# Performance work log

Hardware: AMD Instinct MI355X
Metric: run time of the kernel (lower is better)

The kernel has to match this reference:

```python
import jax, jax.numpy as jnp
from jax import lax
import numpy as np

DN = ('NCHW', 'OIHW', 'NCHW')


def _gaussian_kernel1d(ksize, sigma):
    # torchvision GaussianBlur kernel: linspace-centered, normalized pdf
    x = jnp.linspace(-(ksize - 1) * 0.5, (ksize - 1) * 0.5, ksize, dtype=jnp.float32)
    pdf = jnp.exp(-0.5 * (x / sigma) ** 2)
    return pdf / pdf.sum()


def gaussian_blur(x, ksize, sigma):
    # x: [B, 1, H, W]. Separable blur with reflect padding (== torchvision
    # GaussianBlur, whose 2D kernel is the outer product of the 1D kernel).
    k = _gaussian_kernel1d(ksize, sigma).astype(x.dtype)
    pad = ksize // 2
    xp = jnp.pad(x, ((0, 0), (0, 0), (pad, pad), (pad, pad)), mode='reflect')
    xh = lax.conv_general_dilated(xp, k.reshape(1, 1, ksize, 1), (1, 1), 'VALID',
                                  dimension_numbers=DN)
    return lax.conv_general_dilated(xh, k.reshape(1, 1, 1, ksize), (1, 1), 'VALID',
                                    dimension_numbers=DN)


def _batch_max_norm(x):
    m = jnp.max(x.reshape(x.shape[0], -1), axis=1).reshape(-1, 1, 1, 1)
    return x / m


def _batch_mean_norm(x):
    m = jnp.mean(x.reshape(x.shape[0], -1), axis=1).reshape(-1, 1, 1, 1)
    return x / m


def setup_inputs() -> dict:
    key = jax.random.key(0)
    k1, k2, k3 = jax.random.split(key, 3)
    B, C, H, W = 8, 19, 512, 512
    mask_parse = jax.random.uniform(k1, (B, C, H, W), dtype=jnp.float32)
    area_weights = jax.random.uniform(k2, (C,), dtype=jnp.float32)
    eye_shadows_weight = jax.random.uniform(k3, (1,), dtype=jnp.float32)
    return {"mask_parse": mask_parse, "area_weights": area_weights,
            "eye_shadows_weight": eye_shadows_weight}


def reference(mask_parse, area_weights, eye_shadows_weight):
    background_mask = mask_parse[:, 0:1]          # [B,1,H,W]

    def eye_weight_mask(eyes_mask):
        w = gaussian_blur(eyes_mask, 51, 15.0)
        w = w * (1.0 - eyes_mask) * (1.0 - background_mask)
        return _batch_max_norm(w)

    w_mask_l = eye_weight_mask(mask_parse[:, 4:5])
    w_mask_r = eye_weight_mask(mask_parse[:, 5:6])

    # sum_i mask_parse[:, i] * area_weights[i]
    mask = jnp.einsum('bchw,c->bhw', mask_parse, area_weights)[:, None]
    mask = mask + (w_mask_l + w_mask_r) * eye_shadows_weight
    mask = gaussian_blur(mask, 21, 2.0)
    return _batch_mean_norm(mask)
```

## Files before the change

### kernel.cpp

```cpp
#include <hip/hip_runtime.h>
#include <hip/hip_cooperative_groups.h>

namespace cg = cooperative_groups;

constexpr int B_ = 8, C_ = 19, H_ = 512, W_ = 512;
constexpr int HW_ = H_ * W_;
constexpr int NB = 512;
constexpr int NT = 512;

constexpr int LDSF    = 14880;
constexpr int A_OFF   = 14336;
constexpr int SAW_OFF = 14848;
constexpr int XH_S = 292, T2_OFF = 10512, T2_S = 292, WH_S = 260;
constexpr int ST_S = 540;

__device__ __forceinline__ int refl(int i, int n) {
    i = (i < 0) ? -i : i;
    return (i >= n) ? (2 * n - 2 - i) : i;
}

template<int ND>
__device__ __forceinline__ void gauss_reg(float (&wkr)[ND], float sigma) {
    float s = 0.f;
#pragma unroll
    for (int d = 0; d < ND; ++d) {
        const float t = d / sigma;
        wkr[d] = expf(-0.5f * t * t);
        s += (d ? 2.f : 1.f) * wkr[d];
    }
    const float inv = 1.f / s;
#pragma unroll
    for (int d = 0; d < ND; ++d) wkr[d] *= inv;
}

__device__ __forceinline__ float aweight(int i, const float (&wkr)[11]) {
    float a = 0.f;
#pragma unroll
    for (int t = 0; t < 21; ++t) {
        const float k = wkr[(t < 10) ? (10 - t) : (t - 10)];
        const int o = i + 10 - t;
        if (o >= 0 && o < H_) a += k;
        if (i >= 1 && i <= 10 && t <= 10 - i) a += k;
        if (i >= 501 && i <= 510 && t >= 521 - i) a += k;
    }
    return a;
}


__device__ __forceinline__ void eye_tile(const float* __restrict__ mp,
                                         float* __restrict__ t0,
                                         float* __restrict__ blockmax,
                                         float* __restrict__ eyesumw,
                                         float* lds, int tid, int vb)
{
    float kh[14];
    gauss_reg(kh, 7.5f);
    const int b = vb >> 6, eye = (vb >> 5) & 1, ht = vb & 31;
    const int z = eye * 8 + b;
    const int i0 = ht * 8;
    const float* sb = mp + ((long)b * C_ + 4 + eye) * HW_;

    __syncthreads();
    for (int t = 0; t < 10; ++t) {
        const int e = tid + t * NT;
        if (e < 36 * 142) {
            const int s = e / 142, p = e - s * 142;
            const int R = i0 - 14 + s;
            const long r0 = (long)refl(2 * R, H_) * W_;
            const long r1 = (long)refl(2 * R + 1, H_) * W_;
            const int fc = 4 * p - 28;
            float a0, a1;
            if (fc >= 0 && fc + 3 < W_) {
                const float4 u = *(const float4*)(sb + r0 + fc);
                const float4 v = *(const float4*)(sb + r1 + fc);
                a0 = (u.x + u.y + v.x + v.y) * 0.25f;
                a1 = (u.z + u.w + v.z + v.w) * 0.25f;
            } else {
                const int j0 = 2 * p - 14, j1 = j0 + 1;
                a0 = (sb[r0 + refl(2 * j0, W_)] + sb[r0 + refl(2 * j0 + 1, W_)]
                    + sb[r1 + refl(2 * j0, W_)] + sb[r1 + refl(2 * j0 + 1, W_)]) * 0.25f;
                a1 = (sb[r0 + refl(2 * j1, W_)] + sb[r0 + refl(2 * j1 + 1, W_)]
                    + sb[r1 + refl(2 * j1, W_)] + sb[r1 + refl(2 * j1 + 1, W_)]) * 0.25f;
            }
            *(float2*)(lds + s * XH_S + 2 * p) = make_float2(a0, a1);
        }
    }
    __syncthreads();
    if (tid < 282) {
        float w2[36];
#pragma unroll
        for (int s = 0; s < 36; ++s) w2[s] = lds[s * XH_S + tid + 1];
#pragma unroll
        for (int r = 0; r < 10; ++r) {
            float a = 0.f;
#pragma unroll
            for (int dd = 0; dd < 27; ++dd)
                a = fmaf(w2[r + dd], kh[(dd < 13) ? (13 - dd) : (dd - 13)], a);
            lds[T2_OFF + r * T2_S + tid] = a;
        }
    }
    __syncthreads();
    {
        const int r = tid >> 6, g = tid & 63;
        {
            const float* trow = lds + T2_OFF + r * T2_S + 4 * g;
            float wn[32];
#pragma unroll
            for (int m = 0; m < 8; ++m) {
                const float4 v = *(const float4*)(trow + 4 * m);
                wn[4*m] = v.x; wn[4*m+1] = v.y; wn[4*m+2] = v.z; wn[4*m+3] = v.w;
            }
            float o4[4];
#pragma unroll
            for (int o = 0; o < 4; ++o) {
                float a = 0.f;
#pragma unroll
                for (int dd = 0; dd < 27; ++dd)
                    a = fmaf(wn[o + dd], kh[(dd < 13) ? (13 - dd) : (dd - 13)], a);
                o4[o] = a;
            }
            *(float4*)(lds + r * WH_S + 4 * g) = make_float4(o4[0], o4[1], o4[2], o4[3]);
        }
        if (tid < 128) {
            const int r2 = 8 + (tid >> 6);
            const float* trow = lds + T2_OFF + r2 * T2_S + 4 * g;
            float wn[32];
#pragma unroll
            for (int m = 0; m < 8; ++m) {
                const float4 v = *(const float4*)(trow + 4 * m);
                wn[4*m] = v.x; wn[4*m+1] = v.y; wn[4*m+2] = v.z; wn[4*m+3] = v.w;
            }
            float o4[4];
#pragma unroll
            for (int o = 0; o < 4; ++o) {
                float a = 0.f;
#pragma unroll
                for (int dd = 0; dd < 27; ++dd)
                    a = fmaf(wn[o + dd], kh[(dd < 13) ? (13 - dd) : (dd - 13)], a);
                o4[o] = a;
            }
            *(float4*)(lds + r2 * WH_S + 4 * g) = make_float4(o4[0], o4[1], o4[2], o4[3]);
        }
    }
    __syncthreads();
    const float* A = lds + A_OFF;
    const int c = tid;
    const int j = c >> 1;
    const int jn = (c & 1) ? ((j < 255) ? j + 1 : 255) : ((j > 0) ? j - 1 : 0);
    float cv[10];
#pragma unroll
    for (int s = 0; s < 10; ++s)
        cv[s] = 0.75f * lds[s * WH_S + j] + 0.25f * lds[s * WH_S + jn];
    const float Aw = A[c];
    const long mbase = (long)b * C_ * HW_ + (long)(ht * 16) * W_ + c;
    const float* eyp = mp + mbase + (long)(4 + eye) * HW_;
    const float* bgp = mp + mbase;
    float* db = t0 + (long)z * HW_ + (long)(ht * 16) * W_ + c;
    float vmax = 0.f, vsum = 0.f;
#pragma unroll
    for (int o = 0; o < 16; ++o) {
        const int il = (o >> 1) + 1;
        const int i  = i0 + (o >> 1);
        const float cvn = (o & 1) ? ((i < 255) ? cv[il + 1] : cv[il])
                                  : ((i > 0)   ? cv[il - 1] : cv[il]);
        const float wv = 0.75f * cv[il] + 0.25f * cvn;
        const float ey = eyp[(long)o * W_], bg = bgp[(long)o * W_];
        const float v = wv * (1.f - ey) * (1.f - bg);
        db[(long)o * W_] = v;
        vmax = fmaxf(vmax, v);
        vsum = fmaf(v, A[ht * 16 + o] * Aw, vsum);
    }
#pragma unroll
    for (int off = 32; off; off >>= 1) {
        vmax = fmaxf(vmax, __shfl_down(vmax, off));
        vsum += __shfl_down(vsum, off);
    }
    __syncthreads();
    if ((tid & 63) == 0) { lds[tid >> 6] = vmax; lds[8 + (tid >> 6)] = vsum; }
    __syncthreads();
    if (tid == 0) {
        float m = lds[0], s = lds[8];
        for (int i = 1; i < 8; ++i) { m = fmaxf(m, lds[i]); s += lds[8 + i]; }
        blockmax[z * 32 + ht] = m;
        eyesumw[z * 32 + ht] = s;
    }
}

__device__ __forceinline__ void einsum_part(const float* __restrict__ mp,
                                            float* __restrict__ t3,
                                            float* __restrict__ esum,
                                            float* lds, int tid, int vb)
{
    const float* A   = lds + A_OFF;
    const float* saw = lds + SAW_OFF;
    const int b = vb >> 6, chunk = vb & 63;
    float se = 0.f;
#pragma unroll
    for (int q = 0; q < 2; ++q) {
        const int p4 = chunk * 1024 + q * 512 + tid;
        const long p = (long)p4 * 4;
        const int h = (int)(p >> 9), w0 = (int)(p & 511);
        const float* mpb = mp + (long)b * C_ * HW_ + p;
        float4 acc = make_float4(0.f, 0.f, 0.f, 0.f);
#pragma unroll
        for (int c = 0; c < C_; ++c) {
            const float4 v = *(const float4*)(mpb + (long)c * HW_);
            const float a = saw[c];
            acc.x = fmaf(v.x, a, acc.x);
            acc.y = fmaf(v.y, a, acc.y);
            acc.z = fmaf(v.z, a, acc.z);
            acc.w = fmaf(v.w, a, acc.w);
        }
        *(float4*)(t3 + (long)b * HW_ + p) = acc;
        const float4 a4 = *(const float4*)(A + w0);
        se = fmaf(acc.x * a4.x + acc.y * a4.y + acc.z * a4.z + acc.w * a4.w,
                  A[h], se);
    }
#pragma unroll
    for (int off = 32; off; off >>= 1) se += __shfl_down(se, off);
    __syncthreads();
    if ((tid & 63) == 0) lds[tid >> 6] = se;
    __syncthreads();
    if (tid == 0) {
        float s = 0.f;
        for (int i = 0; i < 8; ++i) s += lds[i];
        esum[vb] = s;
    }
}

__device__ __forceinline__ void phaseB(const float* __restrict__ esw,
                                       const float* __restrict__ t0,
                                       const float* __restrict__ blockmax,
                                       const float* __restrict__ eyesumw,
                                       const float* __restrict__ esum,
                                       float* __restrict__ out,
                                       float* lds, int tid, int vb)
{
    float wkr[11];
    gauss_reg(wkr, 2.f);
    const int b = vb >> 6, tile6 = vb & 63, hb = tile6 * 8;

    float mxL = blockmax[b * 32], mxR = blockmax[(8 + b) * 32];
    float SeL = 0.f, SeR = 0.f, Se = 0.f;
    for (int i = 0; i < 32; ++i) {
        mxL = fmaxf(mxL, blockmax[b * 32 + i]);
        mxR = fmaxf(mxR, blockmax[(8 + b) * 32 + i]);
        SeL += eyesumw[b * 32 + i];
        SeR += eyesumw[(8 + b) * 32 + i];
    }
    for (int i = 0; i < 64; ++i) Se += esum[b * 64 + i];
    const float e = esw[0];
    const float sl = e / mxL, sr = e / mxR;
    const float scale = (float)HW_ / (Se + sl * SeL + sr * SeR);

    const float* t1 = t0 + (long)b * HW_;
    const float* t2 = t0 + (long)(8 + b) * HW_;
    const float* t3 = t0 + (long)(16 + b) * HW_;

    const int c = tid;
    float win[28];
#pragma unroll
    for (int i = 0; i < 28; ++i) {
        const long off = (long)refl(hb - 10 + i, H_) * W_ + c;
        win[i] = fmaf(t1[off], sl, fmaf(t2[off], sr, t3[off]));
    }
    float hv[8];
#pragma unroll
    for (int j = 0; j < 8; ++j) {
        float a = 0.f;
#pragma unroll
        for (int k = 0; k < 21; ++k)
            a = fmaf(win[j + k], wkr[(k < 10) ? (10 - k) : (k - 10)], a);
        hv[j] = a;
    }
    float* st = lds;
#pragma unroll
    for (int j = 0; j < 8; ++j) st[j * ST_S + 12 + c] = hv[j];
    __syncthreads();
    if (tid < 224) {
        const int r = tid / 28, q = tid - r * 28;
        float* srow = st + r * ST_S;
        if (q < 12) srow[11 - q] = srow[13 + q];
        else { const int cc = q - 12; srow[524 + cc] = srow[522 - cc]; }
    }
    __syncthreads();
    const int r = tid >> 6, g = tid & 63, c0 = g * 8;
    const float* srow = st + r * ST_S;
    float wn[32];
#pragma unroll
    for (int m = 0; m < 8; ++m) {
        const float4 v = *(const float4*)(srow + c0 + 4 * m);
        wn[4*m] = v.x; wn[4*m+1] = v.y; wn[4*m+2] = v.z; wn[4*m+3] = v.w;
    }
    float oo[8];
#pragma unroll
    for (int o = 0; o < 8; ++o) {
        float a = 0.f;
#pragma unroll
        for (int k = 0; k < 21; ++k)
            a = fmaf(wn[o + 2 + k], wkr[(k < 10) ? (10 - k) : (k - 10)], a);
        oo[o] = a * scale;
    }
    float* orow = out + (long)b * HW_ + (long)(hb + r) * W_ + c0;
    *(float4*)(orow)     = make_float4(oo[0], oo[1], oo[2], oo[3]);
    *(float4*)(orow + 4) = make_float4(oo[4], oo[5], oo[6], oo[7]);
}

__global__ void __launch_bounds__(NT, 4)
mega_kern(const float* __restrict__ mp, const float* __restrict__ aw,
          const float* __restrict__ esw, float* __restrict__ out,
          float* __restrict__ ws)
{
    cg::grid_group grid = cg::this_grid();
    __shared__ __align__(16) float lds[LDSF];
    const int tid = threadIdx.x, bid = blockIdx.x;
    const int vb = (bid & 7) * 64 + (bid >> 3);
    float* blockmax = ws;
    float* eyesumw  = ws + 512;
    float* esum     = ws + 1024;
    float* t0       = ws + 16384;
    float* t3       = t0 + 16L * HW_;

    {
        float w21[11];
        gauss_reg(w21, 2.f);
        lds[A_OFF + tid] = aweight(tid, w21);
    }
    if (tid < C_) lds[SAW_OFF + tid] = aw[tid];
    __syncthreads();

    if (bid & 1) {
        einsum_part(mp, t3, esum, lds, tid, vb);
        eye_tile(mp, t0, blockmax, eyesumw, lds, tid, vb);
    } else {
        eye_tile(mp, t0, blockmax, eyesumw, lds, tid, vb);
        einsum_part(mp, t3, esum, lds, tid, vb);
    }
    grid.sync();
    phaseB(esw, t0, blockmax, eyesumw, esum, out, lds, tid, vb);
}

__global__ void __launch_bounds__(NT)
fb_A_kern(const float* __restrict__ mp, const float* __restrict__ aw,
          float* __restrict__ ws)
{
    __shared__ __align__(16) float lds[LDSF];
    const int tid = threadIdx.x, bid = blockIdx.x;
    const int vb = (bid & 7) * 64 + (bid >> 3);
    float* blockmax = ws;
    float* eyesumw  = ws + 512;
    float* esum     = ws + 1024;
    float* t0       = ws + 16384;
    float* t3       = t0 + 16L * HW_;
    {
        float w21[11];
        gauss_reg(w21, 2.f);
        lds[A_OFF + tid] = aweight(tid, w21);
    }
    if (tid < C_) lds[SAW_OFF + tid] = aw[tid];
    __syncthreads();
    if (bid & 1) {
        einsum_part(mp, t3, esum, lds, tid, vb);
        eye_tile(mp, t0, blockmax, eyesumw, lds, tid, vb);
    } else {
        eye_tile(mp, t0, blockmax, eyesumw, lds, tid, vb);
        einsum_part(mp, t3, esum, lds, tid, vb);
    }
}

__global__ void __launch_bounds__(NT)
fb_B_kern(const float* __restrict__ esw, float* __restrict__ out,
          float* __restrict__ ws)
{
    __shared__ __align__(16) float lds[LDSF];
    const int tid = threadIdx.x, bid = blockIdx.x;
    const int vb = (bid & 7) * 64 + (bid >> 3);
    phaseB(esw, ws + 16384, ws, ws + 512, ws + 1024, out, lds, tid, vb);
}

extern "C" void kernel_launch(void* const* d_in, const int* in_sizes, int n_in,
                              void* d_out, int out_size, void* d_ws, size_t ws_size,
                              hipStream_t stream)
{
    const float* mp  = (const float*)d_in[0];
    const float* aw  = (const float*)d_in[1];
    const float* esw = (const float*)d_in[2];
    float* out = (float*)d_out;
    float* wsf = (float*)d_ws;

    int coop = 0, nb = 0;
    hipDeviceGetAttribute(&coop, hipDeviceAttributeCooperativeLaunch, 0);
    hipOccupancyMaxActiveBlocksPerMultiprocessor(&nb, (const void*)mega_kern, NT, 0);

    if (coop && nb >= 2) {
        void* args[] = { (void*)&mp, (void*)&aw, (void*)&esw, (void*)&out, (void*)&wsf };
        hipLaunchCooperativeKernel((void*)mega_kern, dim3(NB), dim3(NT), args, 0, stream);
    } else {
        fb_A_kern<<<NB, NT, 0, stream>>>(mp, aw, wsf);
        fb_B_kern<<<NB, NT, 0, stream>>>(esw, out, wsf);
    }
}
```

Before: 51.51 us.

## Double block size to 1024 threads and split per-thread work across halves

```diff
diff --git a/kernel.cpp b/kernel.cpp
--- a/kernel.cpp
+++ b/kernel.cpp
@@ -6,7 +6,7 @@
 constexpr int B_ = 8, C_ = 19, H_ = 512, W_ = 512;
 constexpr int HW_ = H_ * W_;
 constexpr int NB = 512;
-constexpr int NT = 512;
+constexpr int NT = 1024;
 
 constexpr int LDSF    = 14880;
 constexpr int A_OFF   = 14336;
@@ -61,7 +61,7 @@
     const float* sb = mp + ((long)b * C_ + 4 + eye) * HW_;
 
     __syncthreads();
-    for (int t = 0; t < 10; ++t) {
+    for (int t = 0; t < 5; ++t) {
         const int e = tid + t * NT;
         if (e < 36 * 142) {
             const int s = e / 142, p = e - s * 142;
@@ -86,23 +86,26 @@
         }
     }
     __syncthreads();
-    if (tid < 282) {
-        float w2[36];
-#pragma unroll
-        for (int s = 0; s < 36; ++s) w2[s] = lds[s * XH_S + tid + 1];
-#pragma unroll
-        for (int r = 0; r < 10; ++r) {
-            float a = 0.f;
-#pragma unroll
-            for (int dd = 0; dd < 27; ++dd)
-                a = fmaf(w2[r + dd], kh[(dd < 13) ? (13 - dd) : (dd - 13)], a);
-            lds[T2_OFF + r * T2_S + tid] = a;
+    {
+        const int half = tid >> 9, cc = tid & 511;
+        if (cc < 282) {
+            float w2[31];
+#pragma unroll
+            for (int s = 0; s < 31; ++s) w2[s] = lds[(half * 5 + s) * XH_S + cc + 1];
+#pragma unroll
+            for (int r = 0; r < 5; ++r) {
+                float a = 0.f;
+#pragma unroll
+                for (int dd = 0; dd < 27; ++dd)
+                    a = fmaf(w2[r + dd], kh[(dd < 13) ? (13 - dd) : (dd - 13)], a);
+                lds[T2_OFF + (half * 5 + r) * T2_S + cc] = a;
+            }
         }
     }
     __syncthreads();
     {
         const int r = tid >> 6, g = tid & 63;
-        {
+        if (r < 10) {
             const float* trow = lds + T2_OFF + r * T2_S + 4 * g;
             float wn[32];
 #pragma unroll
@@ -121,36 +124,17 @@
             }
             *(float4*)(lds + r * WH_S + 4 * g) = make_float4(o4[0], o4[1], o4[2], o4[3]);
         }
-        if (tid < 128) {
-            const int r2 = 8 + (tid >> 6);
-            const float* trow = lds + T2_OFF + r2 * T2_S + 4 * g;
-            float wn[32];
-#pragma unroll
-            for (int m = 0; m < 8; ++m) {
-                const float4 v = *(const float4*)(trow + 4 * m);
-                wn[4*m] = v.x; wn[4*m+1] = v.y; wn[4*m+2] = v.z; wn[4*m+3] = v.w;
-            }
-            float o4[4];
-#pragma unroll
-            for (int o = 0; o < 4; ++o) {
-                float a = 0.f;
-#pragma unroll
-                for (int dd = 0; dd < 27; ++dd)
-                    a = fmaf(wn[o + dd], kh[(dd < 13) ? (13 - dd) : (dd - 13)], a);
-                o4[o] = a;
-            }
-            *(float4*)(lds + r2 * WH_S + 4 * g) = make_float4(o4[0], o4[1], o4[2], o4[3]);
-        }
     }
     __syncthreads();
     const float* A = lds + A_OFF;
-    const int c = tid;
+    const int c = tid & 511, half = tid >> 9;
     const int j = c >> 1;
     const int jn = (c & 1) ? ((j < 255) ? j + 1 : 255) : ((j > 0) ? j - 1 : 0);
-    float cv[10];
-#pragma unroll
-    for (int s = 0; s < 10; ++s)
-        cv[s] = 0.75f * lds[s * WH_S + j] + 0.25f * lds[s * WH_S + jn];
+    float cv[6];
+#pragma unroll
+    for (int s = 0; s < 6; ++s)
+        cv[s] = 0.75f * lds[(half * 4 + s) * WH_S + j]
+              + 0.25f * lds[(half * 4 + s) * WH_S + jn];
     const float Aw = A[c];
     const long mbase = (long)b * C_ * HW_ + (long)(ht * 16) * W_ + c;
     const float* eyp = mp + mbase + (long)(4 + eye) * HW_;
@@ -158,17 +142,18 @@
     float* db = t0 + (long)z * HW_ + (long)(ht * 16) * W_ + c;
     float vmax = 0.f, vsum = 0.f;
 #pragma unroll
-    for (int o = 0; o < 16; ++o) {
-        const int il = (o >> 1) + 1;
-        const int i  = i0 + (o >> 1);
-        const float cvn = (o & 1) ? ((i < 255) ? cv[il + 1] : cv[il])
-                                  : ((i > 0)   ? cv[il - 1] : cv[il]);
-        const float wv = 0.75f * cv[il] + 0.25f * cvn;
-        const float ey = eyp[(long)o * W_], bg = bgp[(long)o * W_];
+    for (int o = 0; o < 8; ++o) {
+        const int og = half * 8 + o;
+        const int li = (o >> 1) + 1;
+        const int i  = i0 + half * 4 + (o >> 1);
+        const float cvn = (og & 1) ? ((i < 255) ? cv[li + 1] : cv[li])
+                                   : ((i > 0)   ? cv[li - 1] : cv[li]);
+        const float wv = 0.75f * cv[li] + 0.25f * cvn;
+        const float ey = eyp[(long)og * W_], bg = bgp[(long)og * W_];
         const float v = wv * (1.f - ey) * (1.f - bg);
-        db[(long)o * W_] = v;
+        db[(long)og * W_] = v;
         vmax = fmaxf(vmax, v);
-        vsum = fmaf(v, A[ht * 16 + o] * Aw, vsum);
+        vsum = fmaf(v, A[ht * 16 + og] * Aw, vsum);
     }
 #pragma unroll
     for (int off = 32; off; off >>= 1) {
@@ -176,11 +161,11 @@
         vsum += __shfl_down(vsum, off);
     }
     __syncthreads();
-    if ((tid & 63) == 0) { lds[tid >> 6] = vmax; lds[8 + (tid >> 6)] = vsum; }
+    if ((tid & 63) == 0) { lds[tid >> 6] = vmax; lds[16 + (tid >> 6)] = vsum; }
     __syncthreads();
     if (tid == 0) {
-        float m = lds[0], s = lds[8];
-        for (int i = 1; i < 8; ++i) { m = fmaxf(m, lds[i]); s += lds[8 + i]; }
+        float m = lds[0], s = lds[16];
+        for (int i = 1; i < 16; ++i) { m = fmaxf(m, lds[i]); s += lds[16 + i]; }
         blockmax[z * 32 + ht] = m;
         eyesumw[z * 32 + ht] = s;
     }
@@ -194,28 +179,23 @@
     const float* A   = lds + A_OFF;
     const float* saw = lds + SAW_OFF;
     const int b = vb >> 6, chunk = vb & 63;
-    float se = 0.f;
-#pragma unroll
-    for (int q = 0; q < 2; ++q) {
-        const int p4 = chunk * 1024 + q * 512 + tid;
-        const long p = (long)p4 * 4;
-        const int h = (int)(p >> 9), w0 = (int)(p & 511);
-        const float* mpb = mp + (long)b * C_ * HW_ + p;
-        float4 acc = make_float4(0.f, 0.f, 0.f, 0.f);
-#pragma unroll
-        for (int c = 0; c < C_; ++c) {
-            const float4 v = *(const float4*)(mpb + (long)c * HW_);
-            const float a = saw[c];
-            acc.x = fmaf(v.x, a, acc.x);
-            acc.y = fmaf(v.y, a, acc.y);
-            acc.z = fmaf(v.z, a, acc.z);
-            acc.w = fmaf(v.w, a, acc.w);
-        }
-        *(float4*)(t3 + (long)b * HW_ + p) = acc;
-        const float4 a4 = *(const float4*)(A + w0);
-        se = fmaf(acc.x * a4.x + acc.y * a4.y + acc.z * a4.z + acc.w * a4.w,
-                  A[h], se);
-    }
+    const int p4 = chunk * 1024 + tid;
+    const long p = (long)p4 * 4;
+    const int h = (int)(p >> 9), w0 = (int)(p & 511);
+    const float* mpb = mp + (long)b * C_ * HW_ + p;
+    float4 acc = make_float4(0.f, 0.f, 0.f, 0.f);
+#pragma unroll
+    for (int c = 0; c < C_; ++c) {
+        const float4 v = *(const float4*)(mpb + (long)c * HW_);
+        const float a = saw[c];
+        acc.x = fmaf(v.x, a, acc.x);
+        acc.y = fmaf(v.y, a, acc.y);
+        acc.z = fmaf(v.z, a, acc.z);
+        acc.w = fmaf(v.w, a, acc.w);
+    }
+    *(float4*)(t3 + (long)b * HW_ + p) = acc;
+    const float4 a4 = *(const float4*)(A + w0);
+    float se = (acc.x * a4.x + acc.y * a4.y + acc.z * a4.z + acc.w * a4.w) * A[h];
 #pragma unroll
     for (int off = 32; off; off >>= 1) se += __shfl_down(se, off);
     __syncthreads();
@@ -223,7 +203,7 @@
     __syncthreads();
     if (tid == 0) {
         float s = 0.f;
-        for (int i = 0; i < 8; ++i) s += lds[i];
+        for (int i = 0; i < 16; ++i) s += lds[i];
         esum[vb] = s;
     }
 }
@@ -257,16 +237,16 @@
     const float* t2 = t0 + (long)(8 + b) * HW_;
     const float* t3 = t0 + (long)(16 + b) * HW_;
 
-    const int c = tid;
-    float win[28];
-#pragma unroll
-    for (int i = 0; i < 28; ++i) {
-        const long off = (long)refl(hb - 10 + i, H_) * W_ + c;
+    const int c = tid & 511, half = tid >> 9;
+    float win[24];
+#pragma unroll
+    for (int i = 0; i < 24; ++i) {
+        const long off = (long)refl(hb - 10 + half * 4 + i, H_) * W_ + c;
         win[i] = fmaf(t1[off], sl, fmaf(t2[off], sr, t3[off]));
     }
-    float hv[8];
-#pragma unroll
-    for (int j = 0; j < 8; ++j) {
+    float hv[4];
+#pragma unroll
+    for (int j = 0; j < 4; ++j) {
         float a = 0.f;
 #pragma unroll
         for (int k = 0; k < 21; ++k)
@@ -275,7 +255,7 @@
     }
     float* st = lds;
 #pragma unroll
-    for (int j = 0; j < 8; ++j) st[j * ST_S + 12 + c] = hv[j];
+    for (int j = 0; j < 4; ++j) st[(half * 4 + j) * ST_S + 12 + c] = hv[j];
     __syncthreads();
     if (tid < 224) {
         const int r = tid / 28, q = tid - r * 28;
@@ -284,29 +264,28 @@
         else { const int cc = q - 12; srow[524 + cc] = srow[522 - cc]; }
     }
     __syncthreads();
-    const int r = tid >> 6, g = tid & 63, c0 = g * 8;
+    const int r = tid >> 7, g = tid & 127, c0 = g * 4;
     const float* srow = st + r * ST_S;
-    float wn[32];
-#pragma unroll
-    for (int m = 0; m < 8; ++m) {
+    float wn[28];
+#pragma unroll
+    for (int m = 0; m < 7; ++m) {
         const float4 v = *(const float4*)(srow + c0 + 4 * m);
         wn[4*m] = v.x; wn[4*m+1] = v.y; wn[4*m+2] = v.z; wn[4*m+3] = v.w;
     }
-    float oo[8];
-#pragma unroll
-    for (int o = 0; o < 8; ++o) {
+    float oo[4];
+#pragma unroll
+    for (int o = 0; o < 4; ++o) {
         float a = 0.f;
 #pragma unroll
         for (int k = 0; k < 21; ++k)
             a = fmaf(wn[o + 2 + k], wkr[(k < 10) ? (10 - k) : (k - 10)], a);
         oo[o] = a * scale;
     }
-    float* orow = out + (long)b * HW_ + (long)(hb + r) * W_ + c0;
-    *(float4*)(orow)     = make_float4(oo[0], oo[1], oo[2], oo[3]);
-    *(float4*)(orow + 4) = make_float4(oo[4], oo[5], oo[6], oo[7]);
-}
-
-__global__ void __launch_bounds__(NT, 4)
+    *(float4*)(out + (long)b * HW_ + (long)(hb + r) * W_ + c0)
+        = make_float4(oo[0], oo[1], oo[2], oo[3]);
+}
+
+__global__ void __launch_bounds__(NT, 8)
 mega_kern(const float* __restrict__ mp, const float* __restrict__ aw,
           const float* __restrict__ esw, float* __restrict__ out,
           float* __restrict__ ws)
@@ -321,7 +300,7 @@
     float* t0       = ws + 16384;
     float* t3       = t0 + 16L * HW_;
 
-    {
+    if (tid < 512) {
         float w21[11];
         gauss_reg(w21, 2.f);
         lds[A_OFF + tid] = aweight(tid, w21);
@@ -352,7 +331,7 @@
     float* esum     = ws + 1024;
     float* t0       = ws + 16384;
     float* t3       = t0 + 16L * HW_;
-    {
+    if (tid < 512) {
         float w21[11];
         gauss_reg(w21, 2.f);
         lds[A_OFF + tid] = aweight(tid, w21);
```

After: 52.57 us. +2.0%, slower.

## Tile final 21-tap blur into 64x64 2D tiles staged in LDS

Applied to the files above, without the earlier changes.

```diff
diff --git a/kernel.cpp b/kernel.cpp
--- a/kernel.cpp
+++ b/kernel.cpp
@@ -12,7 +12,7 @@
 constexpr int A_OFF   = 14336;
 constexpr int SAW_OFF = 14848;
 constexpr int XH_S = 292, T2_OFF = 10512, T2_S = 292, WH_S = 260;
-constexpr int ST_S = 540;
+constexpr int HB_OFF = 7168;
 
 __device__ __forceinline__ int refl(int i, int n) {
     i = (i < 0) ? -i : i;
@@ -238,7 +238,8 @@
 {
     float wkr[11];
     gauss_reg(wkr, 2.f);
-    const int b = vb >> 6, tile6 = vb & 63, hb = tile6 * 8;
+    const int b = vb >> 6, ty = (vb >> 3) & 7, tx = vb & 7;
+    const int hb = ty * 64, wb = tx * 64;
 
     float mxL = blockmax[b * 32], mxR = blockmax[(8 + b) * 32];
     float SeL = 0.f, SeR = 0.f, Se = 0.f;
@@ -257,53 +258,60 @@
     const float* t2 = t0 + (long)(8 + b) * HW_;
     const float* t3 = t0 + (long)(16 + b) * HW_;
 
-    const int c = tid;
-    float win[28];
-#pragma unroll
-    for (int i = 0; i < 28; ++i) {
-        const long off = (long)refl(hb - 10 + i, H_) * W_ + c;
-        win[i] = fmaf(t1[off], sl, fmaf(t2[off], sr, t3[off]));
-    }
-    float hv[8];
-#pragma unroll
-    for (int j = 0; j < 8; ++j) {
-        float a = 0.f;
-#pragma unroll
-        for (int k = 0; k < 21; ++k)
-            a = fmaf(win[j + k], wkr[(k < 10) ? (10 - k) : (k - 10)], a);
-        hv[j] = a;
-    }
-    float* st = lds;
-#pragma unroll
-    for (int j = 0; j < 8; ++j) st[j * ST_S + 12 + c] = hv[j];
-    __syncthreads();
-    if (tid < 224) {
-        const int r = tid / 28, q = tid - r * 28;
-        float* srow = st + r * ST_S;
-        if (q < 12) srow[11 - q] = srow[13 + q];
-        else { const int cc = q - 12; srow[524 + cc] = srow[522 - cc]; }
-    }
-    __syncthreads();
-    const int r = tid >> 6, g = tid & 63, c0 = g * 8;
-    const float* srow = st + r * ST_S;
-    float wn[32];
-#pragma unroll
-    for (int m = 0; m < 8; ++m) {
-        const float4 v = *(const float4*)(srow + c0 + 4 * m);
-        wn[4*m] = v.x; wn[4*m+1] = v.y; wn[4*m+2] = v.z; wn[4*m+3] = v.w;
-    }
-    float oo[8];
-#pragma unroll
-    for (int o = 0; o < 8; ++o) {
-        float a = 0.f;
-#pragma unroll
-        for (int k = 0; k < 21; ++k)
-            a = fmaf(wn[o + 2 + k], wkr[(k < 10) ? (10 - k) : (k - 10)], a);
-        oo[o] = a * scale;
-    }
-    float* orow = out + (long)b * HW_ + (long)(hb + r) * W_ + c0;
-    *(float4*)(orow)     = make_float4(oo[0], oo[1], oo[2], oo[3]);
-    *(float4*)(orow + 4) = make_float4(oo[4], oo[5], oo[6], oo[7]);
+    float* stage = lds;
+    for (int e2 = tid; e2 < 84 * 84; e2 += NT) {
+        const int r = e2 / 84, c = e2 - r * 84;
+        const long off = (long)refl(hb - 10 + r, H_) * W_ + refl(wb - 10 + c, W_);
+        stage[r * 85 + c] = fmaf(t1[off], sl, fmaf(t2[off], sr, t3[off]));
+    }
+    __syncthreads();
+
+    float* hbuf = lds + HB_OFF;
+    if (tid < 504) {
+        const int c = tid % 84, g = tid / 84;
+        const int r0 = g * 11;
+        float wn[31];
+#pragma unroll
+        for (int s = 0; s < 31; ++s) {
+            const int rr = r0 + s;
+            wn[s] = (rr < 84) ? stage[rr * 85 + c] : 0.f;
+        }
+#pragma unroll
+        for (int j = 0; j < 11; ++j) {
+            const int r = r0 + j;
+            if (r < 64) {
+                float a = 0.f;
+#pragma unroll
+                for (int k = 0; k < 21; ++k)
+                    a = fmaf(wn[j + k], wkr[(k < 10) ? (10 - k) : (k - 10)], a);
+                hbuf[r * 84 + c] = a;
+            }
+        }
+    }
+    __syncthreads();
+
+    {
+        const int r = tid >> 3, i = tid & 7;
+        const float* hrow = hbuf + r * 84 + 8 * i;
+        float wn[28];
+#pragma unroll
+        for (int m = 0; m < 7; ++m) {
+            const float4 v = *(const float4*)(hrow + 4 * m);
+            wn[4*m] = v.x; wn[4*m+1] = v.y; wn[4*m+2] = v.z; wn[4*m+3] = v.w;
+        }
+        float oo[8];
+#pragma unroll
+        for (int o = 0; o < 8; ++o) {
+            float a = 0.f;
+#pragma unroll
+            for (int k = 0; k < 21; ++k)
+                a = fmaf(wn[o + k], wkr[(k < 10) ? (10 - k) : (k - 10)], a);
+            oo[o] = a * scale;
+        }
+        float* orow = out + (long)b * HW_ + (long)(hb + r) * W_ + wb + 8 * i;
+        *(float4*)(orow)     = make_float4(oo[0], oo[1], oo[2], oo[3]);
+        *(float4*)(orow + 4) = make_float4(oo[4], oo[5], oo[6], oo[7]);
+    }
 }
 
 __global__ void __launch_bounds__(NT, 4)
```

Measured after the change: 53.04 us. 3.0% more time.

## Store low-res eye blur and recompute eye weights in phase B

Applied to the files above, without the earlier changes.

```diff
diff --git a/kernel.cpp b/kernel.cpp
--- a/kernel.cpp
+++ b/kernel.cpp
@@ -12,7 +12,13 @@
 constexpr int A_OFF   = 14336;
 constexpr int SAW_OFF = 14848;
 constexpr int XH_S = 292, T2_OFF = 10512, T2_S = 292, WH_S = 260;
-constexpr int ST_S = 540;
+constexpr int WHL_OFF = 0, WHR_OFF = 4680, ST_OFF = 9360, ST_S = 540;
+
+constexpr long WS_BM   = 0;
+constexpr long WS_EW   = 512;
+constexpr long WS_ESUM = 1024;
+constexpr long WS_WH   = 4096;
+constexpr long WS_T3   = WS_WH + 16L * 256 * 256;
 
 __device__ __forceinline__ int refl(int i, int n) {
     i = (i < 0) ? -i : i;
@@ -46,9 +52,8 @@
     return a;
 }
 
-
 __device__ __forceinline__ void eye_tile(const float* __restrict__ mp,
-                                         float* __restrict__ t0,
+                                         float* __restrict__ whg,
                                          float* __restrict__ blockmax,
                                          float* __restrict__ eyesumw,
                                          float* lds, int tid, int vb)
@@ -119,7 +124,10 @@
                     a = fmaf(wn[o + dd], kh[(dd < 13) ? (13 - dd) : (dd - 13)], a);
                 o4[o] = a;
             }
-            *(float4*)(lds + r * WH_S + 4 * g) = make_float4(o4[0], o4[1], o4[2], o4[3]);
+            const float4 ov = make_float4(o4[0], o4[1], o4[2], o4[3]);
+            *(float4*)(lds + r * WH_S + 4 * g) = ov;
+            if (r >= 1)
+                *(float4*)(whg + (long)z * 65536 + (long)(i0 + r - 1) * 256 + 4 * g) = ov;
         }
         if (tid < 128) {
             const int r2 = 8 + (tid >> 6);
@@ -139,7 +147,10 @@
                     a = fmaf(wn[o + dd], kh[(dd < 13) ? (13 - dd) : (dd - 13)], a);
                 o4[o] = a;
             }
-            *(float4*)(lds + r2 * WH_S + 4 * g) = make_float4(o4[0], o4[1], o4[2], o4[3]);
+            const float4 ov = make_float4(o4[0], o4[1], o4[2], o4[3]);
+            *(float4*)(lds + r2 * WH_S + 4 * g) = ov;
+            if (r2 == 8)
+                *(float4*)(whg + (long)z * 65536 + (long)(i0 + 7) * 256 + 4 * g) = ov;
         }
     }
     __syncthreads();
@@ -155,7 +166,6 @@
     const long mbase = (long)b * C_ * HW_ + (long)(ht * 16) * W_ + c;
     const float* eyp = mp + mbase + (long)(4 + eye) * HW_;
     const float* bgp = mp + mbase;
-    float* db = t0 + (long)z * HW_ + (long)(ht * 16) * W_ + c;
     float vmax = 0.f, vsum = 0.f;
 #pragma unroll
     for (int o = 0; o < 16; ++o) {
@@ -166,7 +176,6 @@
         const float wv = 0.75f * cv[il] + 0.25f * cvn;
         const float ey = eyp[(long)o * W_], bg = bgp[(long)o * W_];
         const float v = wv * (1.f - ey) * (1.f - bg);
-        db[(long)o * W_] = v;
         vmax = fmaxf(vmax, v);
         vsum = fmaf(v, A[ht * 16 + o] * Aw, vsum);
     }
@@ -228,8 +237,10 @@
     }
 }
 
-__device__ __forceinline__ void phaseB(const float* __restrict__ esw,
-                                       const float* __restrict__ t0,
+__device__ __forceinline__ void phaseB(const float* __restrict__ mp,
+                                       const float* __restrict__ esw,
+                                       const float* __restrict__ whg,
+                                       const float* __restrict__ t3g,
                                        const float* __restrict__ blockmax,
                                        const float* __restrict__ eyesumw,
                                        const float* __restrict__ esum,
@@ -253,29 +264,58 @@
     const float sl = e / mxL, sr = e / mxR;
     const float scale = (float)HW_ / (Se + sl * SeL + sr * SeR);
 
-    const float* t1 = t0 + (long)b * HW_;
-    const float* t2 = t0 + (long)(8 + b) * HW_;
-    const float* t3 = t0 + (long)(16 + b) * HW_;
-
+    int sb0 = ((hb - 10) >> 1) - 1;
+    sb0 = sb0 < 0 ? 0 : (sb0 > 238 ? 238 : sb0);
+    const float* whgL = whg + (long)b * 65536;
+    const float* whgR = whg + (long)(8 + b) * 65536;
+    float* whL = lds + WHL_OFF;
+    float* whR = lds + WHR_OFF;
+    for (int e2 = tid; e2 < 18 * 64; e2 += NT) {
+        const int r = e2 >> 6, g4 = e2 & 63;
+        *(float4*)(whL + r * 260 + 4 * g4)
+            = *(const float4*)(whgL + (long)(sb0 + r) * 256 + 4 * g4);
+        *(float4*)(whR + r * 260 + 4 * g4)
+            = *(const float4*)(whgR + (long)(sb0 + r) * 256 + 4 * g4);
+    }
+    __syncthreads();
+
+    const float* mp0 = mp + (long)b * C_ * HW_;
+    const float* t3b = t3g + (long)b * HW_;
     const int c = tid;
-    float win[28];
+    const int j = c >> 1;
+    const int jn = (c & 1) ? ((j < 255) ? j + 1 : 255) : ((j > 0) ? j - 1 : 0);
+
+    float hv[8] = {0.f, 0.f, 0.f, 0.f, 0.f, 0.f, 0.f, 0.f};
 #pragma unroll
     for (int i = 0; i < 28; ++i) {
-        const long off = (long)refl(hb - 10 + i, H_) * W_ + c;
-        win[i] = fmaf(t1[off], sl, fmaf(t2[off], sr, t3[off]));
-    }
-    float hv[8];
-#pragma unroll
-    for (int j = 0; j < 8; ++j) {
-        float a = 0.f;
-#pragma unroll
-        for (int k = 0; k < 21; ++k)
-            a = fmaf(win[j + k], wkr[(k < 10) ? (10 - k) : (k - 10)], a);
-        hv[j] = a;
-    }
-    float* st = lds;
-#pragma unroll
-    for (int j = 0; j < 8; ++j) st[j * ST_S + 12 + c] = hv[j];
+        const int Rr = refl(hb - 10 + i, H_);
+        const int irow = Rr >> 1;
+        const int irn = (Rr & 1) ? ((irow < 255) ? irow + 1 : irow)
+                                 : ((irow > 0) ? irow - 1 : irow);
+        const int la = irow - sb0, lb = irn - sb0;
+        const float cvLa = 0.75f * whL[la * 260 + j] + 0.25f * whL[la * 260 + jn];
+        const float cvLb = 0.75f * whL[lb * 260 + j] + 0.25f * whL[lb * 260 + jn];
+        const float wvL = 0.75f * cvLa + 0.25f * cvLb;
+        const float cvRa = 0.75f * whR[la * 260 + j] + 0.25f * whR[la * 260 + jn];
+        const float cvRb = 0.75f * whR[lb * 260 + j] + 0.25f * whR[lb * 260 + jn];
+        const float wvR = 0.75f * cvRa + 0.25f * cvRb;
+        const long po = (long)Rr * W_ + c;
+        const float ch0 = mp0[po];
+        const float ch4 = mp0[po + 4L * HW_];
+        const float ch5 = mp0[po + 5L * HW_];
+        const float vL = wvL * (1.f - ch4) * (1.f - ch0);
+        const float vR = wvR * (1.f - ch5) * (1.f - ch0);
+        const float win = fmaf(vL, sl, fmaf(vR, sr, t3b[po]));
+#pragma unroll
+        for (int j2 = 0; j2 < 8; ++j2) {
+            const int k = i - j2;
+            if (k >= 0 && k < 21)
+                hv[j2] = fmaf(win, wkr[(k < 10) ? (10 - k) : (k - 10)], hv[j2]);
+        }
+    }
+    float* st = lds + ST_OFF;
+#pragma unroll
+    for (int j2 = 0; j2 < 8; ++j2) st[j2 * ST_S + 12 + c] = hv[j2];
     __syncthreads();
     if (tid < 224) {
         const int r = tid / 28, q = tid - r * 28;
@@ -284,26 +324,28 @@
         else { const int cc = q - 12; srow[524 + cc] = srow[522 - cc]; }
     }
     __syncthreads();
-    const int r = tid >> 6, g = tid & 63, c0 = g * 8;
-    const float* srow = st + r * ST_S;
-    float wn[32];
-#pragma unroll
-    for (int m = 0; m < 8; ++m) {
-        const float4 v = *(const float4*)(srow + c0 + 4 * m);
-        wn[4*m] = v.x; wn[4*m+1] = v.y; wn[4*m+2] = v.z; wn[4*m+3] = v.w;
-    }
-    float oo[8];
-#pragma unroll
-    for (int o = 0; o < 8; ++o) {
-        float a = 0.f;
-#pragma unroll
-        for (int k = 0; k < 21; ++k)
-            a = fmaf(wn[o + 2 + k], wkr[(k < 10) ? (10 - k) : (k - 10)], a);
-        oo[o] = a * scale;
-    }
-    float* orow = out + (long)b * HW_ + (long)(hb + r) * W_ + c0;
-    *(float4*)(orow)     = make_float4(oo[0], oo[1], oo[2], oo[3]);
-    *(float4*)(orow + 4) = make_float4(oo[4], oo[5], oo[6], oo[7]);
+    {
+        const int r = tid >> 6, g = tid & 63, c0 = g * 8;
+        const float* srow = st + r * ST_S;
+        float wn[32];
+#pragma unroll
+        for (int m = 0; m < 8; ++m) {
+            const float4 v = *(const float4*)(srow + c0 + 4 * m);
+            wn[4*m] = v.x; wn[4*m+1] = v.y; wn[4*m+2] = v.z; wn[4*m+3] = v.w;
+        }
+        float oo[8];
+#pragma unroll
+        for (int o = 0; o < 8; ++o) {
+            float a = 0.f;
+#pragma unroll
+            for (int k = 0; k < 21; ++k)
+                a = fmaf(wn[o + 2 + k], wkr[(k < 10) ? (10 - k) : (k - 10)], a);
+            oo[o] = a * scale;
+        }
+        float* orow = out + (long)b * HW_ + (long)(hb + r) * W_ + c0;
+        *(float4*)(orow)     = make_float4(oo[0], oo[1], oo[2], oo[3]);
+        *(float4*)(orow + 4) = make_float4(oo[4], oo[5], oo[6], oo[7]);
+    }
 }
 
 __global__ void __launch_bounds__(NT, 4)
@@ -315,11 +357,11 @@
     __shared__ __align__(16) float lds[LDSF];
     const int tid = threadIdx.x, bid = blockIdx.x;
     const int vb = (bid & 7) * 64 + (bid >> 3);
-    float* blockmax = ws;
-    float* eyesumw  = ws + 512;
-    float* esum     = ws + 1024;
-    float* t0       = ws + 16384;
-    float* t3       = t0 + 16L * HW_;
+    float* blockmax = ws + WS_BM;
+    float* eyesumw  = ws + WS_EW;
+    float* esum     = ws + WS_ESUM;
+    float* whg      = ws + WS_WH;
+    float* t3       = ws + WS_T3;
 
     {
         float w21[11];
@@ -331,13 +373,13 @@
 
     if (bid & 1) {
         einsum_part(mp, t3, esum, lds, tid, vb);
-        eye_tile(mp, t0, blockmax, eyesumw, lds, tid, vb);
+        eye_tile(mp, whg, blockmax, eyesumw, lds, tid, vb);
     } else {
-        eye_tile(mp, t0, blockmax, eyesumw, lds, tid, vb);
+        eye_tile(mp, whg, blockmax, eyesumw, lds, tid, vb);
         einsum_part(mp, t3, esum, lds, tid, vb);
     }
     grid.sync();
-    phaseB(esw, t0, blockmax, eyesumw, esum, out, lds, tid, vb);
+    phaseB(mp, esw, whg, t3, blockmax, eyesumw, esum, out, lds, tid, vb);
 }
 
 __global__ void __launch_bounds__(NT)
@@ -347,11 +389,11 @@
     __shared__ __align__(16) float lds[LDSF];
     const int tid = threadIdx.x, bid = blockIdx.x;
     const int vb = (bid & 7) * 64 + (bid >> 3);
-    float* blockmax = ws;
-    float* eyesumw  = ws + 512;
-    float* esum     = ws + 1024;
-    float* t0       = ws + 16384;
-    float* t3       = t0 + 16L * HW_;
+    float* blockmax = ws + WS_BM;
+    float* eyesumw  = ws + WS_EW;
+    float* esum     = ws + WS_ESUM;
+    float* whg      = ws + WS_WH;
+    float* t3       = ws + WS_T3;
     {
         float w21[11];
         gauss_reg(w21, 2.f);
@@ -361,21 +403,24 @@
     __syncthreads();
     if (bid & 1) {
         einsum_part(mp, t3, esum, lds, tid, vb);
-        eye_tile(mp, t0, blockmax, eyesumw, lds, tid, vb);
+        eye_tile(mp, whg, blockmax, eyesumw, lds, tid, vb);
     } else {
-        eye_tile(mp, t0, blockmax, eyesumw, lds, tid, vb);
+        eye_tile(mp, whg, blockmax, eyesumw, lds, tid, vb);
         einsum_part(mp, t3, esum, lds, tid, vb);
     }
 }
 
 __global__ void __launch_bounds__(NT)
-fb_B_kern(const float* __restrict__ esw, float* __restrict__ out,
-          float* __restrict__ ws)
+fb_B_kern(const float* __restrict__ mp, const float* __restrict__ esw,
+          float* __restrict__ out, float* __restrict__ ws)
 {
     __shared__ __align__(16) float lds[LDSF];
     const int tid = threadIdx.x, bid = blockIdx.x;
     const int vb = (bid & 7) * 64 + (bid >> 3);
-    phaseB(esw, ws + 16384, ws, ws + 512, ws + 1024, out, lds, tid, vb);
+    {
+    }
+    phaseB(mp, esw, ws + WS_WH, ws + WS_T3, ws + WS_BM, ws + WS_EW,
+           ws + WS_ESUM, out, lds, tid, vb);
 }
 
 extern "C" void kernel_launch(void* const* d_in, const int* in_sizes, int n_in,
@@ -397,6 +442,6 @@
         hipLaunchCooperativeKernel((void*)mega_kern, dim3(NB), dim3(NT), args, 0, stream);
     } else {
         fb_A_kern<<<NB, NT, 0, stream>>>(mp, aw, wsf);
-        fb_B_kern<<<NB, NT, 0, stream>>>(esw, out, wsf);
-    }
-}
+        fb_B_kern<<<NB, NT, 0, stream>>>(mp, esw, out, wsf);
+    }
+}
```

After: 57.23 us. 1.11x slower.
